# Performance work log

Measured on AMD Instinct MI355X. Metric: run time of the kernel, lower is better.

The kernel has to match this reference:

```python
import jax, jax.numpy as jnp
import numpy as np

# Module constants from __init__: z_max=32, ppm=2 -> delta=0.5, z_min=delta=0.5, log_prob=True
Z_MIN = 0.5
Z_MAX = 32.0
DELTA = 0.5


def _depth_positions(S):
    # depth_steps = arange(z_min, z_max + delta, delta) -> Z=64 bins in [0.5, 32]
    depth_steps = jnp.arange(Z_MIN, Z_MAX + DELTA, DELTA)
    log_steps = jnp.log2(depth_steps)
    log_min = np.log2(Z_MIN)
    log_max = np.log2(Z_MAX)
    norm = (log_steps - log_min) / (log_max - log_min)  # in [0, 1]
    # grid_sample align_corners=True maps [-1,1] -> [0, S-1]; norm*2-1 -> norm*(S-1)
    return norm * (S - 1)  # (Z,)


def setup_inputs() -> dict:
    key = jax.random.key(0)
    k1, k2 = jax.random.split(key)
    image = jax.random.normal(k1, (32, 64, 64, 128), dtype=jnp.float32)          # (B,D,H,W)
    polar_log_depths = jax.random.normal(k2, (32, 64, 128, 64), dtype=jnp.float32)  # (B,H,W,S)
    return {"image": image, "polar_log_depths": polar_log_depths}


def reference(image, polar_log_depths):
    S = polar_log_depths.shape[-1]
    pos = _depth_positions(S)                                 # (Z,) fixed interp positions
    i0 = jnp.clip(jnp.floor(pos).astype(jnp.int32), 0, S - 1)
    i1 = jnp.clip(i0 + 1, 0, S - 1)
    w = pos - i0.astype(pos.dtype)                            # linear weights; w=0 at right edge
    v0 = jnp.take(polar_log_depths, i0, axis=-1)              # (B,H,W,Z)
    v1 = jnp.take(polar_log_depths, i1, axis=-1)
    depth_scores = v0 * (1.0 - w) + v1 * w                    # 1D linear interp == grid_sample here

    # log_prob=True branch: softmax / logsumexp over height axis (dim=1)
    depth_prob = jax.nn.softmax(depth_scores, axis=1)         # (B,H,W,Z)
    cell_score = jax.nn.logsumexp(depth_scores, axis=1)       # (B,W,Z)

    # einsum '...dhw,...hwz->...dzw': weighted reduction over height
    image_polar = jnp.einsum('bdhw,bhwz->bdzw', image, depth_prob)  # (B,D,Z,W)
    return image_polar, cell_score
```

## Files before the change

kernel.cpp:

```cpp
#include <hip/hip_runtime.h>
#include <hip/hip_bf16.h>
#include <math.h>

#define B_ 32
#define D_ 64
#define H_ 64
#define W_ 128
#define S_ 64
#define Z_ 64
#define WT 8

typedef __attribute__((ext_vector_type(8))) short bf16x8;
typedef __attribute__((ext_vector_type(4))) float f32x4;

static __device__ __forceinline__ short f2bf(float f) {
    union { __hip_bfloat16 h; short s; } u;
    u.h = __float2bfloat16(f);
    return u.s;
}

static __device__ __forceinline__ int swz(int w, int row, int oct) {
    return w * 8192 + row * 128 + (((oct ^ row ^ w) & 7) << 4);
}
static __device__ __forceinline__ int swz0(int row, int oct) {
    return row * 128 + (((oct ^ row) & 7) << 4);
}

__global__ __launch_bounds__(1024, 4)
void polar_proj_kernel(const float* __restrict__ image,
                       const float* __restrict__ polar,
                       float* __restrict__ out_img,
                       float* __restrict__ out_cell) {
    __shared__ __align__(16) unsigned char sP[WT * 8192];
    __shared__ __align__(16) unsigned char sA[WT * 8192];
    __shared__ __align__(16) unsigned char sWz[8192];

    const int t = threadIdx.x;

    const int cpx = gridDim.x >> 3;
    const int logical = (blockIdx.x & 7) * cpx + (blockIdx.x >> 3);
    const int b  = logical >> 4;
    const int w0 = (logical & 15) << 3;

    const int wq = t & 1;
    float4 ir[8];
#pragma unroll
    for (int i = 0; i < 8; ++i) {
        const int p = i * 512 + (t >> 1);
        const int d = p >> 6, h = p & 63;
        ir[i] = *(const float4*)(image + ((size_t)((b * D_ + d) * H_ + h)) * W_ + w0 + wq * 4);
    }

    const int q4 = t & 3;
    const int rbase = t >> 2;
    float4 pr[8];
#pragma unroll
    for (int rp = 0; rp < 2; ++rp) {
        const int rr = rbase + rp * 256;
        const int w = rr >> 6, h = rr & 63;
        const float* src = polar + ((size_t)((b * H_ + h) * W_ + w0 + w)) * S_ + q4 * 16;
#pragma unroll
        for (int k = 0; k < 4; ++k)
            pr[rp * 4 + k] = *(const float4*)(src + k * 4);
    }

    {
        const int z  = t >> 4;
        const int s4 = (t & 15) << 2;
        const float posf = (log2f(0.5f + 0.5f * (float)z) + 1.0f) * 10.5f;
        int i0 = (int)floorf(posf);
        i0 = i0 < 0 ? 0 : (i0 > S_ - 1 ? S_ - 1 : i0);
        const int i1 = (i0 + 1 > S_ - 1) ? (S_ - 1) : (i0 + 1);
        const float wz = posf - (float)i0;
        short e4[4];
#pragma unroll
        for (int c = 0; c < 4; ++c) {
            const int s = s4 + c;
            float v = 0.0f;
            if (s == i0) v += 1.0f - wz;
            if (s == i1) v += wz;
            e4[c] = f2bf(v);
        }
        int2 pk;
        pk.x = (e4[0] & 0xffff) | (e4[1] << 16);
        pk.y = (e4[2] & 0xffff) | (e4[3] << 16);
        *(int2*)(sWz + swz0(z, s4 >> 3) + ((s4 & 7) << 1)) = pk;
    }

#pragma unroll
    for (int i = 0; i < 8; ++i) {
        const int p = i * 512 + (t >> 1);
        const int d = p >> 6, h = p & 63;
#pragma unroll
        for (int c = 0; c < 4; ++c) {
            const int w = wq * 4 + c;
            *(short*)(sA + swz(w, d, h >> 3) + ((h & 7) << 1)) = f2bf(((const float*)&ir[i])[c]);
        }
    }

#pragma unroll
    for (int rp = 0; rp < 2; ++rp) {
        const int rr = rbase + rp * 256;
        const int w = rr >> 6, h = rr & 63;
#pragma unroll
        for (int c = 0; c < 2; ++c) {
            bf16x8 v;
#pragma unroll
            for (int e = 0; e < 8; ++e)
                v[e] = f2bf(((const float*)&pr[rp * 4 + c * 2 + (e >> 2)])[e & 3]);
            *(bf16x8*)(sP + swz(w, h, q4 * 2 + c)) = v;
        }
    }
    __syncthreads();

    const int lane = t & 63;
    const int wv   = t >> 6;
    const int fr   = lane & 15, lg = lane >> 4;
    const int wS   = wv >> 1, zh = wv & 1;

    f32x4 sacc[4][2] = {};
#pragma unroll
    for (int ks = 0; ks < 2; ++ks) {
        const bf16x8 bf0 = *(const bf16x8*)(sWz + swz0(zh * 32 + fr,      ks * 4 + lg));
        const bf16x8 bf1 = *(const bf16x8*)(sWz + swz0(zh * 32 + 16 + fr, ks * 4 + lg));
#pragma unroll
        for (int mt = 0; mt < 4; ++mt) {
            const bf16x8 a = *(const bf16x8*)(sP + swz(wS, mt * 16 + fr, ks * 4 + lg));
            sacc[mt][0] = __builtin_amdgcn_mfma_f32_16x16x32_bf16(a, bf0, sacc[mt][0], 0, 0, 0);
            sacc[mt][1] = __builtin_amdgcn_mfma_f32_16x16x32_bf16(a, bf1, sacc[mt][1], 0, 0, 0);
        }
    }

    float ex[4][2][4];
    float ss0 = 0.0f, ss1 = 0.0f;
#pragma unroll
    for (int mt = 0; mt < 4; ++mt)
#pragma unroll
        for (int r = 0; r < 4; ++r) {
            const float e0 = __expf(sacc[mt][0][r]);
            const float e1 = __expf(sacc[mt][1][r]);
            ex[mt][0][r] = e0;
            ex[mt][1][r] = e1;
            ss0 += e0;
            ss1 += e1;
        }
    ss0 += __shfl_xor(ss0, 16);
    ss0 += __shfl_xor(ss0, 32);
    ss1 += __shfl_xor(ss1, 16);
    ss1 += __shfl_xor(ss1, 32);
    if (lg == 0) {
        float* oc = out_cell + ((size_t)b * W_ + w0 + wS) * Z_ + zh * 32 + fr;
        oc[0]  = __logf(ss0);
        oc[16] = __logf(ss1);
    }
    const float inv0 = 1.0f / ss0;
    const float inv1 = 1.0f / ss1;
    __syncthreads();

#pragma unroll
    for (int nt = 0; nt < 2; ++nt) {
        const int zrow = zh * 32 + nt * 16 + fr;
        const float inv = nt ? inv1 : inv0;
#pragma unroll
        for (int mt = 0; mt < 4; ++mt) {
            const short p0 = f2bf(ex[mt][nt][0] * inv);
            const short p1 = f2bf(ex[mt][nt][1] * inv);
            const short p2 = f2bf(ex[mt][nt][2] * inv);
            const short p3 = f2bf(ex[mt][nt][3] * inv);
            int2 pk;
            pk.x = (p0 & 0xffff) | (p1 << 16);
            pk.y = (p2 & 0xffff) | (p3 << 16);
            *(int2*)(sP + swz(wS, zrow, mt * 2 + (lg >> 1)) + ((lg & 1) << 3)) = pk;
        }
    }
    __syncthreads();

    const int mtp = wv >> 2, ntp = wv & 3;
    const int rowA = mtp * 16 + fr;
    const int rowB = ntp * 16 + fr;
    f32x4 acc[8] = {};
#pragma unroll
    for (int w = 0; w < 8; ++w)
#pragma unroll
        for (int ks = 0; ks < 2; ++ks) {
            const bf16x8 a  = *(const bf16x8*)(sA + swz(w, rowA, ks * 4 + lg));
            const bf16x8 bb = *(const bf16x8*)(sP + swz(w, rowB, ks * 4 + lg));
            acc[w] = __builtin_amdgcn_mfma_f32_16x16x32_bf16(a, bb, acc[w], 0, 0, 0);
        }
    __syncthreads();

    unsigned char* rg = (wv & 8) ? (sA + (wv & 7) * 8192) : (sP + (wv & 7) * 8192);
#pragma unroll
    for (int r = 0; r < 4; ++r) {
        const int li = fr * 4 + lg + r * 64;
#pragma unroll
        for (int wp = 0; wp < 4; ++wp) {
            float2 v;
            v.x = acc[wp * 2][r];
            v.y = acc[wp * 2 + 1][r];
            *(float2*)(rg + li * 32 + wp * 8) = v;
        }
    }
    __syncthreads();
    const unsigned char* rgc = rg;
#pragma unroll
    for (int i = 0; i < 8; ++i) {
        const int dz = (lane >> 1) + i * 32;
        const int wh = lane & 1;
        const int di = dz >> 4, zi = dz & 15;
        const int li = zi * 4 + (di >> 2) + (di & 3) * 64;
        const float4 v = *(const float4*)(rgc + li * 32 + wh * 16);
        const int d = mtp * 16 + di;
        const int z = ntp * 16 + zi;
        *(float4*)(out_img + ((size_t)((b * D_ + d) * Z_) + z) * W_ + w0 + wh * 4) = v;
    }
}

extern "C" void kernel_launch(void* const* d_in, const int* in_sizes, int n_in,
                              void* d_out, int out_size, void* d_ws, size_t ws_size,
                              hipStream_t stream) {
    const float* image = (const float*)d_in[0];
    const float* polar = (const float*)d_in[1];
    float* out_img  = (float*)d_out;
    float* out_cell = out_img + (size_t)B_ * D_ * Z_ * W_;
    dim3 grid(B_ * (W_ / WT));
    polar_proj_kernel<<<grid, 1024, 0, stream>>>(image, polar, out_img, out_cell);
}
```

Baseline: 51.97 us.

## Halve W tile per block, compute interp weights in registers, store output directly

Shrinks the per-block W tile from 8 to 4 columns with 512 threads, so there are twice as many blocks and half the LDS per block. The interpolation weight matrix is now built directly in registers instead of being staged through a shared buffer. The second GEMM is remapped so each lane holds four consecutive w values for a (d,z) pair and writes float4 outputs straight to global memory, which removes the LDS transpose round-trip and its two barriers. The trade-off is 16-byte output stores that are less contiguous per row, and repeated per-lane weight computation.

```diff
diff --git a/kernel.cpp b/kernel.cpp
--- a/kernel.cpp
+++ b/kernel.cpp
@@ -8,7 +8,7 @@
 #define W_ 128
 #define S_ 64
 #define Z_ 64
-#define WT 8
+#define WT 4
 
 typedef __attribute__((ext_vector_type(8))) short bf16x8;
 typedef __attribute__((ext_vector_type(4))) float f32x4;
@@ -18,96 +18,81 @@
     u.h = __float2bfloat16(f);
     return u.s;
 }
+static __device__ __forceinline__ float getc(const float4& v, int k) {
+    switch (k) { case 0: return v.x; case 1: return v.y; case 2: return v.z; default: return v.w; }
+}
 
 static __device__ __forceinline__ int swz(int w, int row, int oct) {
     return w * 8192 + row * 128 + (((oct ^ row ^ w) & 7) << 4);
 }
-static __device__ __forceinline__ int swz0(int row, int oct) {
-    return row * 128 + (((oct ^ row) & 7) << 4);
-}
-
-__global__ __launch_bounds__(1024, 4)
+
+__global__ __launch_bounds__(512, 4)
 void polar_proj_kernel(const float* __restrict__ image,
                        const float* __restrict__ polar,
                        float* __restrict__ out_img,
                        float* __restrict__ out_cell) {
     __shared__ __align__(16) unsigned char sP[WT * 8192];
     __shared__ __align__(16) unsigned char sA[WT * 8192];
-    __shared__ __align__(16) unsigned char sWz[8192];
 
     const int t = threadIdx.x;
 
     const int cpx = gridDim.x >> 3;
     const int logical = (blockIdx.x & 7) * cpx + (blockIdx.x >> 3);
-    const int b  = logical >> 4;
-    const int w0 = (logical & 15) << 3;
-
-    const int wq = t & 1;
-    float4 ir[8];
-#pragma unroll
-    for (int i = 0; i < 8; ++i) {
-        const int p = i * 512 + (t >> 1);
-        const int d = p >> 6, h = p & 63;
-        ir[i] = *(const float4*)(image + ((size_t)((b * D_ + d) * H_ + h)) * W_ + w0 + wq * 4);
+    const int b  = logical >> 5;
+    const int w0 = (logical & 31) << 2;
+
+    float4 ir[2][4];
+#pragma unroll
+    for (int i = 0; i < 2; ++i) {
+        const int g  = i * 512 + t;
+        const int d  = g >> 4;
+        const int h0 = (g & 15) << 2;
+#pragma unroll
+        for (int k = 0; k < 4; ++k)
+            ir[i][k] = *(const float4*)(image + ((size_t)((b * D_ + d) * H_ + h0 + k)) * W_ + w0);
     }
 
     const int q4 = t & 3;
     const int rbase = t >> 2;
-    float4 pr[8];
+    float4 pr[2][4];
 #pragma unroll
     for (int rp = 0; rp < 2; ++rp) {
-        const int rr = rbase + rp * 256;
+        const int rr = rp * 128 + rbase;
         const int w = rr >> 6, h = rr & 63;
         const float* src = polar + ((size_t)((b * H_ + h) * W_ + w0 + w)) * S_ + q4 * 16;
 #pragma unroll
         for (int k = 0; k < 4; ++k)
-            pr[rp * 4 + k] = *(const float4*)(src + k * 4);
-    }
-
-    {
-        const int z  = t >> 4;
-        const int s4 = (t & 15) << 2;
-        const float posf = (log2f(0.5f + 0.5f * (float)z) + 1.0f) * 10.5f;
-        int i0 = (int)floorf(posf);
-        i0 = i0 < 0 ? 0 : (i0 > S_ - 1 ? S_ - 1 : i0);
-        const int i1 = (i0 + 1 > S_ - 1) ? (S_ - 1) : (i0 + 1);
-        const float wz = posf - (float)i0;
-        short e4[4];
-#pragma unroll
-        for (int c = 0; c < 4; ++c) {
-            const int s = s4 + c;
-            float v = 0.0f;
-            if (s == i0) v += 1.0f - wz;
-            if (s == i1) v += wz;
-            e4[c] = f2bf(v);
-        }
-        int2 pk;
-        pk.x = (e4[0] & 0xffff) | (e4[1] << 16);
-        pk.y = (e4[2] & 0xffff) | (e4[3] << 16);
-        *(int2*)(sWz + swz0(z, s4 >> 3) + ((s4 & 7) << 1)) = pk;
-    }
-
-#pragma unroll
-    for (int i = 0; i < 8; ++i) {
-        const int p = i * 512 + (t >> 1);
-        const int d = p >> 6, h = p & 63;
-#pragma unroll
-        for (int c = 0; c < 4; ++c) {
-            const int w = wq * 4 + c;
-            *(short*)(sA + swz(w, d, h >> 3) + ((h & 7) << 1)) = f2bf(((const float*)&ir[i])[c]);
+            pr[rp][k] = *(const float4*)(src + k * 4);
+    }
+
+#pragma unroll
+    for (int i = 0; i < 2; ++i) {
+        const int g  = i * 512 + t;
+        const int d  = g >> 4;
+        const int h0 = (g & 15) << 2;
+#pragma unroll
+        for (int w = 0; w < 4; ++w) {
+            const short s0 = f2bf(getc(ir[i][0], w));
+            const short s1 = f2bf(getc(ir[i][1], w));
+            const short s2 = f2bf(getc(ir[i][2], w));
+            const short s3 = f2bf(getc(ir[i][3], w));
+            int2 pk;
+            pk.x = (s0 & 0xffff) | (s1 << 16);
+            pk.y = (s2 & 0xffff) | (s3 << 16);
+            *(int2*)(sA + swz(w, d, h0 >> 3) + ((h0 & 7) << 1)) = pk;
         }
     }
 
 #pragma unroll
     for (int rp = 0; rp < 2; ++rp) {
-        const int rr = rbase + rp * 256;
+        const int rr = rp * 128 + rbase;
         const int w = rr >> 6, h = rr & 63;
 #pragma unroll
         for (int c = 0; c < 2; ++c) {
             bf16x8 v;
 #pragma unroll
             for (int e = 0; e < 8; ++e)
-                v[e] = f2bf(((const float*)&pr[rp * 4 + c * 2 + (e >> 2)])[e & 3]);
+                v[e] = f2bf(getc(pr[rp][c * 2 + (e >> 2)], e & 3));
             *(bf16x8*)(sP + swz(w, h, q4 * 2 + c)) = v;
         }
     }
@@ -118,18 +103,42 @@
     const int fr   = lane & 15, lg = lane >> 4;
     const int wS   = wv >> 1, zh = wv & 1;
 
+    int   i0_[2];
+    float wz_[2];
+#pragma unroll
+    for (int nt = 0; nt < 2; ++nt) {
+        const int z = zh * 32 + nt * 16 + fr;
+        const float posf = (log2f(0.5f + 0.5f * (float)z) + 1.0f) * 10.5f;
+        int i0 = (int)floorf(posf);
+        i0 = i0 < 0 ? 0 : (i0 > S_ - 1 ? S_ - 1 : i0);
+        i0_[nt] = i0;
+        wz_[nt] = posf - (float)i0;
+    }
+    bf16x8 bw[2][2];
+#pragma unroll
+    for (int ks = 0; ks < 2; ++ks)
+#pragma unroll
+        for (int nt = 0; nt < 2; ++nt) {
+            const int i0 = i0_[nt];
+            const int i1 = (i0 + 1 > S_ - 1) ? (S_ - 1) : (i0 + 1);
+            const float wz = wz_[nt];
+#pragma unroll
+            for (int e = 0; e < 8; ++e) {
+                const int s = ks * 32 + lg * 8 + e;
+                const float v = (s == i0 ? 1.0f - wz : 0.0f) + (s == i1 ? wz : 0.0f);
+                bw[ks][nt][e] = f2bf(v);
+            }
+        }
+
     f32x4 sacc[4][2] = {};
 #pragma unroll
-    for (int ks = 0; ks < 2; ++ks) {
-        const bf16x8 bf0 = *(const bf16x8*)(sWz + swz0(zh * 32 + fr,      ks * 4 + lg));
-        const bf16x8 bf1 = *(const bf16x8*)(sWz + swz0(zh * 32 + 16 + fr, ks * 4 + lg));
+    for (int ks = 0; ks < 2; ++ks)
 #pragma unroll
         for (int mt = 0; mt < 4; ++mt) {
             const bf16x8 a = *(const bf16x8*)(sP + swz(wS, mt * 16 + fr, ks * 4 + lg));
-            sacc[mt][0] = __builtin_amdgcn_mfma_f32_16x16x32_bf16(a, bf0, sacc[mt][0], 0, 0, 0);
-            sacc[mt][1] = __builtin_amdgcn_mfma_f32_16x16x32_bf16(a, bf1, sacc[mt][1], 0, 0, 0);
-        }
-    }
+            sacc[mt][0] = __builtin_amdgcn_mfma_f32_16x16x32_bf16(a, bw[ks][0], sacc[mt][0], 0, 0, 0);
+            sacc[mt][1] = __builtin_amdgcn_mfma_f32_16x16x32_bf16(a, bw[ks][1], sacc[mt][1], 0, 0, 0);
+        }
 
     float ex[4][2][4];
     float ss0 = 0.0f, ss1 = 0.0f;
@@ -175,45 +184,34 @@
     }
     __syncthreads();
 
-    const int mtp = wv >> 2, ntp = wv & 3;
+    const int mtp = wv >> 1, ntp = wv & 1;
     const int rowA = mtp * 16 + fr;
-    const int rowB = ntp * 16 + fr;
-    f32x4 acc[8] = {};
-#pragma unroll
-    for (int w = 0; w < 8; ++w)
+    f32x4 acc[4][2] = {};
+#pragma unroll
+    for (int w = 0; w < 4; ++w)
 #pragma unroll
         for (int ks = 0; ks < 2; ++ks) {
-            const bf16x8 a  = *(const bf16x8*)(sA + swz(w, rowA, ks * 4 + lg));
-            const bf16x8 bb = *(const bf16x8*)(sP + swz(w, rowB, ks * 4 + lg));
-            acc[w] = __builtin_amdgcn_mfma_f32_16x16x32_bf16(a, bb, acc[w], 0, 0, 0);
-        }
-    __syncthreads();
-
-    unsigned char* rg = (wv & 8) ? (sA + (wv & 7) * 8192) : (sP + (wv & 7) * 8192);
-#pragma unroll
-    for (int r = 0; r < 4; ++r) {
-        const int li = fr * 4 + lg + r * 64;
-#pragma unroll
-        for (int wp = 0; wp < 4; ++wp) {
-            float2 v;
-            v.x = acc[wp * 2][r];
-            v.y = acc[wp * 2 + 1][r];
-            *(float2*)(rg + li * 32 + wp * 8) = v;
-        }
-    }
-    __syncthreads();
-    const unsigned char* rgc = rg;
-#pragma unroll
-    for (int i = 0; i < 8; ++i) {
-        const int dz = (lane >> 1) + i * 32;
-        const int wh = lane & 1;
-        const int di = dz >> 4, zi = dz & 15;
-        const int li = zi * 4 + (di >> 2) + (di & 3) * 64;
-        const float4 v = *(const float4*)(rgc + li * 32 + wh * 16);
-        const int d = mtp * 16 + di;
-        const int z = ntp * 16 + zi;
-        *(float4*)(out_img + ((size_t)((b * D_ + d) * Z_) + z) * W_ + w0 + wh * 4) = v;
-    }
+            const bf16x8 a = *(const bf16x8*)(sA + swz(w, rowA, ks * 4 + lg));
+#pragma unroll
+            for (int zz = 0; zz < 2; ++zz) {
+                const bf16x8 bb = *(const bf16x8*)(sP + swz(w, ntp * 32 + zz * 16 + fr, ks * 4 + lg));
+                acc[w][zz] = __builtin_amdgcn_mfma_f32_16x16x32_bf16(a, bb, acc[w][zz], 0, 0, 0);
+            }
+        }
+
+#pragma unroll
+    for (int zz = 0; zz < 2; ++zz)
+#pragma unroll
+        for (int r = 0; r < 4; ++r) {
+            const int d = mtp * 16 + lg * 4 + r;
+            const int z = ntp * 32 + zz * 16 + fr;
+            float4 o;
+            o.x = acc[0][zz][r];
+            o.y = acc[1][zz][r];
+            o.z = acc[2][zz][r];
+            o.w = acc[3][zz][r];
+            *(float4*)(out_img + ((size_t)((b * D_ + d) * Z_) + z) * W_ + w0) = o;
+        }
 }
 
 extern "C" void kernel_launch(void* const* d_in, const int* in_sizes, int n_in,
@@ -224,5 +222,5 @@
     float* out_img  = (float*)d_out;
     float* out_cell = out_img + (size_t)B_ * D_ * Z_ * W_;
     dim3 grid(B_ * (W_ / WT));
-    polar_proj_kernel<<<grid, 1024, 0, stream>>>(image, polar, out_img, out_cell);
-}
+    polar_proj_kernel<<<grid, 512, 0, stream>>>(image, polar, out_img, out_cell);
+}
```

Measured after the change: 51.99 us. About the same (+0.0%).
